# Kernel tuning notes

Hardware: AMD Instinct MI355X
Metric: run time of the kernel (lower is better)

## Reference

```python
import jax, jax.numpy as jnp
import numpy as np

HEADS = 16
HEAD_DIM = 64
DIM = 1024
INNER = HEADS * HEAD_DIM
EPS = 1e-5


def setup_inputs() -> dict:
    key = jax.random.key(0)
    ks = jax.random.split(key, 7)
    s_qkv = (2.0 / (DIM + 3 * INNER)) ** 0.5
    s_out = (2.0 / (INNER + DIM)) ** 0.5
    return {
        "x": jax.random.normal(ks[0], (4, 2048, DIM), dtype=jnp.float32),
        "w_qkv": jax.random.normal(ks[1], (DIM, 3 * INNER), dtype=jnp.float32) * s_qkv,
        "b_qkv": jnp.zeros((3 * INNER,), dtype=jnp.float32),
        "w_out": jax.random.normal(ks[2], (INNER, DIM), dtype=jnp.float32) * s_out,
        "b_out": jnp.zeros((DIM,), dtype=jnp.float32),
        "ln_gamma": jnp.ones((DIM,), dtype=jnp.float32),
        "ln_beta": jnp.zeros((DIM,), dtype=jnp.float32),
    }


def reference(x, w_qkv, b_qkv, w_out, b_out, ln_gamma, ln_beta):
    # Pre-norm LayerNorm
    mu = jnp.mean(x, axis=-1, keepdims=True)
    var = jnp.var(x, axis=-1, keepdims=True)
    xn = (x - mu) * jax.lax.rsqrt(var + EPS) * ln_gamma + ln_beta
    # QKV projection: [b, l, 3*inner]
    qkv = xn @ w_qkv + b_qkv
    q, k, v = jnp.split(qkv, 3, axis=-1)
    b, l, _ = x.shape
    def heads(t):  # [b, l, inner] -> [b, h, l, d]
        return t.reshape(b, l, HEADS, HEAD_DIM).transpose(0, 2, 1, 3)
    q, k, v = heads(q), heads(k), heads(v)
    scale = HEAD_DIM ** -0.5
    scores = jnp.einsum('bhqd,bhkd->bhqk', q, k) * scale
    att = jax.nn.softmax(scores, axis=-1)
    out = jnp.einsum('bhqk,bhkd->bhqd', att, v)
    out = out.transpose(0, 2, 1, 3).reshape(b, l, INNER)
    return out @ w_out + b_out
```

## Files before the change

### kernel.cpp

```cpp
#include <hip/hip_runtime.h>
#include <stdint.h>

typedef __bf16 bf16;
typedef bf16 bf16x4 __attribute__((ext_vector_type(4)));
typedef bf16 bf16x8 __attribute__((ext_vector_type(8)));
typedef float f32x4 __attribute__((ext_vector_type(4)));


__device__ __forceinline__ void gll16(const bf16* g, const bf16* l) {
  __builtin_amdgcn_global_load_lds(
      (__attribute__((address_space(1))) void*)(g),
      (__attribute__((address_space(3))) void*)(l),
      16, 0, 0);
}

__global__ __launch_bounds__(256) void ln_kernel(
    const float* __restrict__ x, const float* __restrict__ gamma,
    const float* __restrict__ beta, bf16* __restrict__ xn)
{
  __shared__ float red[8];
  const long row = blockIdx.x;
  const int t = threadIdx.x;
  f32x4 f = *(const f32x4*)(x + row * 1024 + t * 4);
  float sum = f[0] + f[1] + f[2] + f[3];
  float sq  = f[0]*f[0] + f[1]*f[1] + f[2]*f[2] + f[3]*f[3];
#pragma unroll
  for (int sh = 1; sh < 64; sh <<= 1) {
    sum += __shfl_xor(sum, sh, 64);
    sq  += __shfl_xor(sq,  sh, 64);
  }
  const int wave = t >> 6, lane = t & 63;
  if (lane == 0) { red[wave] = sum; red[wave + 4] = sq; }
  __syncthreads();
  sum = red[0] + red[1] + red[2] + red[3];
  sq  = red[4] + red[5] + red[6] + red[7];
  const float mu  = sum * (1.0f / 1024.0f);
  const float var = sq * (1.0f / 1024.0f) - mu * mu;
  const float rs  = rsqrtf(var + 1e-5f);
  f32x4 g = *(const f32x4*)(gamma + t * 4);
  f32x4 bb = *(const f32x4*)(beta + t * 4);
  bf16x4 ov;
#pragma unroll
  for (int i = 0; i < 4; i++)
    ov[i] = (bf16)((f[i] - mu) * rs * g[i] + bb[i]);
  *(bf16x4*)(xn + row * 1024 + t * 4) = ov;
}

__global__ __launch_bounds__(256) void transpose2_kernel(
    const float* __restrict__ wqkv, bf16* __restrict__ wqkvT,
    const float* __restrict__ wout, bf16* __restrict__ woutT)
{
  __shared__ bf16 tile[32][33];
  const int bx = blockIdx.x;
  const float* in;
  bf16* out;
  int Cc, c0;
  if (bx < 96) { in = wqkv; out = wqkvT; Cc = 3072; c0 = bx * 32; }
  else         { in = wout; out = woutT; Cc = 1024; c0 = (bx - 96) * 32; }
  const int r0 = blockIdx.y * 32;
  const int tx = threadIdx.x & 31, ty = threadIdx.x >> 5;
#pragma unroll
  for (int i = 0; i < 32; i += 8)
    tile[ty + i][tx] = (bf16)in[(long)(r0 + ty + i) * Cc + c0 + tx];
  __syncthreads();
#pragma unroll
  for (int i = 0; i < 32; i += 8)
    out[(long)(c0 + ty + i) * 1024 + r0 + tx] = tile[tx][ty + i];
}

__global__ __launch_bounds__(256, 3) void gemm_bt(
    const bf16* __restrict__ A, const bf16* __restrict__ BT,
    const float* __restrict__ bias, float* __restrict__ C,
    bf16* __restrict__ qb, bf16* __restrict__ kb, bf16* __restrict__ vtb,
    int K, int N, int mode)
{
  __shared__ bf16 sA[3][128 * 32];
  __shared__ bf16 sB[3][128 * 32];
  const int t = threadIdx.x;
  const int lane = t & 63;
  const int wave = t >> 6;
  const int wave_u = __builtin_amdgcn_readfirstlane(wave);
  const int quad = lane >> 4;
  const int c16 = lane & 15;
  const int wm = (wave >> 1) * 64;
  const int wn = (wave & 1) * 64;
  const int m0 = blockIdx.x * 128;
  const int n0 = blockIdx.y * 128;

  f32x4 acc[4][4] = {};

  const int srow = t >> 2;
  const int scol = (((t & 3) ^ ((t >> 3) & 3)) * 8);
  const bf16* gA = A + (long)(m0 + srow) * K + scol;
  const bf16* gB = BT + (long)(n0 + srow) * K + scol;
  const long rowskip = (long)64 * K;
  const int ksw = (quad ^ ((c16 >> 1) & 3)) * 8;

  const int S = K >> 5;

  auto stage = [&](int b, int kk) {
    const bf16* lA = sA[0] + b * 4096 + wave_u * 512;
    const bf16* lB = sB[0] + b * 4096 + wave_u * 512;
    const int k0 = kk * 32;
    gll16(gA + k0, lA);
    gll16(gA + k0 + rowskip, lA + 2048);
    gll16(gB + k0, lB);
    gll16(gB + k0 + rowskip, lB + 2048);
  };

  stage(0, 0);
  stage(1, 1);

  int bcur = 0;
  for (int s = 0; s < S; s++) {
    if (s + 2 < S) {
      const int bnx = (bcur >= 1) ? bcur - 1 : 2;
      stage(bnx, s + 2);
      asm volatile("s_waitcnt vmcnt(8)" ::: "memory");
    } else if (s + 1 < S) {
      asm volatile("s_waitcnt vmcnt(4)" ::: "memory");
    } else {
      asm volatile("s_waitcnt vmcnt(0)" ::: "memory");
    }
    __builtin_amdgcn_s_barrier();

    const bf16* cA = sA[0] + bcur * 4096;
    const bf16* cB = sB[0] + bcur * 4096;
    bf16x8 af[4], bfr[4];
#pragma unroll
    for (int i = 0; i < 4; i++)
      af[i] = *(const bf16x8*)(cA + (wm + i * 16 + c16) * 32 + ksw);
#pragma unroll
    for (int j = 0; j < 4; j++)
      bfr[j] = *(const bf16x8*)(cB + (wn + j * 16 + c16) * 32 + ksw);
#pragma unroll
    for (int i = 0; i < 4; i++)
#pragma unroll
      for (int j = 0; j < 4; j++)
        acc[i][j] = __builtin_amdgcn_mfma_f32_16x16x32_bf16(af[i], bfr[j], acc[i][j], 0, 0, 0);

    __builtin_amdgcn_s_barrier();
    bcur = (bcur == 2) ? 0 : bcur + 1;
  }

#pragma unroll
  for (int i = 0; i < 4; i++) {
    const int mbase = m0 + wm + i * 16 + quad * 4;
#pragma unroll
    for (int j = 0; j < 4; j++) {
      const int n = n0 + wn + j * 16 + c16;
      const float bv = bias[n];
      if (mode == 0) {
#pragma unroll
        for (int r = 0; r < 4; r++)
          C[(long)(mbase + r) * N + n] = acc[i][j][r] + bv;
      } else {
        const int part = n >> 10;
        const int inner = n & 1023;
        const int h = inner >> 6, d = inner & 63;
#pragma unroll
        for (int r = 0; r < 4; r++) {
          const int m = mbase + r;
          const int b = m >> 11, l = m & 2047;
          const long bh = (long)((b << 4) | h);
          const float v = acc[i][j][r] + bv;
          if (part == 0)      qb [(bh * 2048 + l) * 64 + d] = (bf16)(v * 0.18033688f);
          else if (part == 1) kb [(bh * 2048 + l) * 64 + d] = (bf16)v;
          else                vtb[(bh * 64 + d) * 2048 + l] = (bf16)v;
        }
      }
    }
  }
}

__global__ __launch_bounds__(256, 2) void attn_kernel(
    const bf16* __restrict__ q, const bf16* __restrict__ k,
    const bf16* __restrict__ vt, bf16* __restrict__ att)
{
  __shared__ bf16 sK[128 * 68];
  __shared__ bf16 sVt[64 * 132];

  const int i = blockIdx.x;
  const int xcd = i & 7;
  const int wi = i >> 3;
  const int qt = wi & 7;
  const int bh = xcd * 8 + (wi >> 3);
  const int b = bh >> 4, h = bh & 15;
  const int q0 = qt * 256;
  const int t = threadIdx.x;
  const int wave = t >> 6, lane = t & 63;
  const int quad = lane >> 4, c16 = lane & 15;

  const bf16* qp = q + (long)bh * (2048 * 64);
  const bf16* kp = k + (long)bh * (2048 * 64);
  const bf16* vp = vt + (long)bh * (64 * 2048);

  bf16x8 aq[4][2];
#pragma unroll
  for (int m = 0; m < 4; m++) {
    const bf16* qrow = qp + (long)(q0 + wave * 64 + m * 16 + c16) * 64 + quad * 8;
    aq[m][0] = *(const bf16x8*)(qrow);
    aq[m][1] = *(const bf16x8*)(qrow + 32);
  }

  f32x4 o_acc[4][4] = {};
  f32x4 o_sum[4] = {};
  bf16x8 vones;
#pragma unroll
  for (int z = 0; z < 8; z++) vones[z] = (bf16)1.0f;

  const int kr = t >> 3;
  const int kd = (t & 7) * 8;
  const int vr = t >> 4;
  const int vc = t & 15;
  const int vl = vc * 8;
  const int vD0 = (vc >> 2) * 32 + (vc & 1) * 16 + ((vc >> 1) & 1) * 4;

  bf16x8 kreg[4], vreg[4];
#pragma unroll
  for (int it = 0; it < 4; it++) {
    kreg[it] = *(const bf16x8*)(kp + (long)(it * 32 + kr) * 64 + kd);
    vreg[it] = *(const bf16x8*)(vp + (long)(it * 16 + vr) * 2048 + vl);
  }

  for (int kt = 0; kt < 16; kt++) {
    __syncthreads();
#pragma unroll
    for (int it = 0; it < 4; it++)
      *(bf16x8*)&sK[(it * 32 + kr) * 68 + kd] = kreg[it];
#pragma unroll
    for (int it = 0; it < 4; it++) {
      const bf16x8 v = vreg[it];
      const bf16x4 lo = __builtin_shufflevector(v, v, 0, 1, 2, 3);
      const bf16x4 hi = __builtin_shufflevector(v, v, 4, 5, 6, 7);
      bf16* d = &sVt[(it * 16 + vr) * 132 + vD0];
      *(bf16x4*)(d)     = lo;
      *(bf16x4*)(d + 8) = hi;
    }
    __syncthreads();

    const int kvn = ((kt + 1) & 15) * 128;

#pragma unroll
    for (int ks = 0; ks < 4; ks++) {
      bf16x8 ap[4];
#pragma unroll
      for (int e = 0; e < 2; e++) {
        const int jb = ks * 2 + e;
        const bf16x8 bk0 = *(const bf16x8*)&sK[(jb * 16 + c16) * 68 + quad * 8];
        const bf16x8 bk1 = *(const bf16x8*)&sK[(jb * 16 + c16) * 68 + 32 + quad * 8];
#pragma unroll
        for (int m = 0; m < 4; m++) {
          f32x4 z = {};
          z = __builtin_amdgcn_mfma_f32_16x16x32_bf16(bk0, aq[m][0], z, 0, 0, 0);
          z = __builtin_amdgcn_mfma_f32_16x16x32_bf16(bk1, aq[m][1], z, 0, 0, 0);
#pragma unroll
          for (int r = 0; r < 4; r++)
            ap[m][e * 4 + r] = (bf16)__builtin_amdgcn_exp2f(z[r]);
        }
      }
      if (ks == 1) {
#pragma unroll
        for (int it = 0; it < 4; it++)
          kreg[it] = *(const bf16x8*)(kp + (long)(kvn + it * 32 + kr) * 64 + kd);
      }
      if (ks == 2) {
#pragma unroll
        for (int it = 0; it < 4; it++)
          vreg[it] = *(const bf16x8*)(vp + (long)(it * 16 + vr) * 2048 + kvn + vl);
      }
#pragma unroll
      for (int m = 0; m < 4; m++)
        o_sum[m] = __builtin_amdgcn_mfma_f32_16x16x32_bf16(ap[m], vones, o_sum[m], 0, 0, 0);
#pragma unroll
      for (int jd = 0; jd < 4; jd++) {
        const bf16x8 bv = *(const bf16x8*)&sVt[(jd * 16 + c16) * 132 + ks * 32 + quad * 8];
#pragma unroll
        for (int m = 0; m < 4; m++)
          o_acc[m][jd] = __builtin_amdgcn_mfma_f32_16x16x32_bf16(ap[m], bv, o_acc[m][jd], 0, 0, 0);
      }
    }
  }

#pragma unroll
  for (int m = 0; m < 4; m++) {
#pragma unroll
    for (int r = 0; r < 4; r++) {
      const float inv = 1.0f / o_sum[m][r];
      const long rowbase = ((long)b * 2048 + q0 + wave * 64 + m * 16 + quad * 4 + r) * 1024 + h * 64;
#pragma unroll
      for (int jd = 0; jd < 4; jd++)
        att[rowbase + jd * 16 + c16] = (bf16)(o_acc[m][jd][r] * inv);
    }
  }
}

extern "C" void kernel_launch(void* const* d_in, const int* in_sizes, int n_in,
                              void* d_out, int out_size, void* d_ws, size_t ws_size,
                              hipStream_t stream) {
  (void)in_sizes; (void)n_in; (void)out_size; (void)ws_size;
  const float* x     = (const float*)d_in[0];
  const float* w_qkv = (const float*)d_in[1];
  const float* b_qkv = (const float*)d_in[2];
  const float* w_out = (const float*)d_in[3];
  const float* b_out = (const float*)d_in[4];
  const float* gamma = (const float*)d_in[5];
  const float* beta  = (const float*)d_in[6];
  float* out = (float*)d_out;
  bf16* ws  = (bf16*)d_ws;

  bf16* xn    = ws;
  bf16* wqkvT = ws + 8388608;
  bf16* woutT = wqkvT + 3145728;
  bf16* qbuf  = woutT + 1048576;
  bf16* kbuf  = qbuf + 8388608;
  bf16* vtbuf = kbuf + 8388608;
  bf16* att   = xn;

  transpose2_kernel<<<dim3(128, 32), 256, 0, stream>>>(w_qkv, wqkvT, w_out, woutT);
  ln_kernel<<<dim3(8192), 256, 0, stream>>>(x, gamma, beta, xn);
  gemm_bt<<<dim3(8192 / 128, 3072 / 128), 256, 0, stream>>>(
      xn, wqkvT, b_qkv, (float*)nullptr, qbuf, kbuf, vtbuf, 1024, 3072, 1);
  attn_kernel<<<dim3(512), 256, 0, stream>>>(qbuf, kbuf, vtbuf, att);
  gemm_bt<<<dim3(8192 / 128, 1024 / 128), 256, 0, stream>>>(
      att, woutT, b_out, out, (bf16*)nullptr, (bf16*)nullptr, (bf16*)nullptr, 1024, 1024, 0);
}
```

Baseline: 272.5 us.

## Add 256x256-tile 8-wave QKV GEMM with interleaved staging and MFMA scheduling

Replaces the 128x128 QKV projection GEMM with a dedicated kernel that uses 256x256 block tiles, 512 threads and a K-tile of 64. Global-to-LDS loads are double-buffered and interleaved with quarter-tile MFMA groups under explicit barriers, waitcnts and setprio. The aim is more operand reuse per LDS byte and better overlap of loads with matrix math. In exchange the grid shrinks to 384 blocks, the schedule is intricate to get right, and the scattered q/k/vT epilogue stores are unchanged.

```diff
diff --git a/kernel.cpp b/kernel.cpp
--- a/kernel.cpp
+++ b/kernel.cpp
@@ -71,8 +71,7 @@
 __global__ __launch_bounds__(256, 3) void gemm_bt(
     const bf16* __restrict__ A, const bf16* __restrict__ BT,
     const float* __restrict__ bias, float* __restrict__ C,
-    bf16* __restrict__ qb, bf16* __restrict__ kb, bf16* __restrict__ vtb,
-    int K, int N, int mode)
+    int K, int N)
 {
   __shared__ bf16 sA[3][128 * 32];
   __shared__ bf16 sB[3][128 * 32];
@@ -150,27 +149,168 @@
     for (int j = 0; j < 4; j++) {
       const int n = n0 + wn + j * 16 + c16;
       const float bv = bias[n];
-      if (mode == 0) {
-#pragma unroll
-        for (int r = 0; r < 4; r++)
-          C[(long)(mbase + r) * N + n] = acc[i][j][r] + bv;
-      } else {
-        const int part = n >> 10;
-        const int inner = n & 1023;
-        const int h = inner >> 6, d = inner & 63;
-#pragma unroll
-        for (int r = 0; r < 4; r++) {
-          const int m = mbase + r;
-          const int b = m >> 11, l = m & 2047;
-          const long bh = (long)((b << 4) | h);
-          const float v = acc[i][j][r] + bv;
-          if (part == 0)      qb [(bh * 2048 + l) * 64 + d] = (bf16)(v * 0.18033688f);
-          else if (part == 1) kb [(bh * 2048 + l) * 64 + d] = (bf16)v;
-          else                vtb[(bh * 64 + d) * 2048 + l] = (bf16)v;
-        }
+#pragma unroll
+      for (int r = 0; r < 4; r++)
+        C[(long)(mbase + r) * N + n] = acc[i][j][r] + bv;
+    }
+  }
+}
+
+__global__ __launch_bounds__(512, 2) void gemm_qkv256(
+    const bf16* __restrict__ A, const bf16* __restrict__ BT,
+    const float* __restrict__ bias,
+    bf16* __restrict__ qb, bf16* __restrict__ kb, bf16* __restrict__ vtb,
+    int K, int N)
+{
+  __shared__ bf16 sA[2][2][128 * 64];
+  __shared__ bf16 sB[2][2][128 * 64];
+  const int t = threadIdx.x;
+  const int lane = t & 63;
+  const int wave = t >> 6;
+  const int wave_u = __builtin_amdgcn_readfirstlane(wave);
+  const int quad = lane >> 4, c16 = lane & 15;
+  const int wM = wave >> 2;
+  const int wN = wave & 3;
+  const int wm = wM * 128;
+  const int wn = wN * 64;
+  const int m0 = blockIdx.x * 256;
+  const int n0 = blockIdx.y * 256;
+  const int NT = K >> 6;
+  const int NI = K >> 7;
+
+  f32x4 acc[8][4] = {};
+
+  const int sr = t >> 3;
+  const int scol = ((t & 7) ^ (sr & 7)) * 8;
+  const int fsw = c16 & 7;
+
+  auto stageA = [&](int buf, int half, int tile) {
+    const long kc = (long)tile * 64;
+    const long rb = (long)(m0 + half * 128);
+    const bf16* l = &sA[buf][half][0] + wave_u * 512;
+    gll16(A + (rb + sr) * K + kc + scol, l);
+    gll16(A + (rb + 64 + sr) * K + kc + scol, l + 4096);
+  };
+  auto stageB = [&](int buf, int half, int tile) {
+    const long kc = (long)tile * 64;
+    const long rb = (long)(n0 + half * 128);
+    const bf16* l = &sB[buf][half][0] + wave_u * 512;
+    gll16(BT + (rb + sr) * K + kc + scol, l);
+    gll16(BT + (rb + 64 + sr) * K + kc + scol, l + 4096);
+  };
+
+  bf16x8 af[4][2], bfr[4][2];
+  auto loadA = [&](int b, int mh) {
+#pragma unroll
+    for (int mi = 0; mi < 4; mi++) {
+      const int lr = (mh * 4 + mi) * 16 + c16;
+#pragma unroll
+      for (int ks = 0; ks < 2; ks++)
+        af[mi][ks] = *(const bf16x8*)&sA[b][wM][lr * 64 + (((ks * 4 + quad) ^ fsw) * 8)];
+    }
+  };
+  auto loadB = [&](int b) {
+#pragma unroll
+    for (int ni = 0; ni < 4; ni++) {
+      const int lr = (wN & 1) * 64 + ni * 16 + c16;
+#pragma unroll
+      for (int ks = 0; ks < 2; ks++)
+        bfr[ni][ks] = *(const bf16x8*)&sB[b][wN >> 1][lr * 64 + (((ks * 4 + quad) ^ fsw) * 8)];
+    }
+  };
+
+#define QUADMFMA(MH, NH)                                                      \
+  __builtin_amdgcn_s_setprio(1);                                              \
+  _Pragma("unroll")                                                           \
+  for (int mi = 0; mi < 4; mi++)                                              \
+    _Pragma("unroll")                                                         \
+    for (int ni = 0; ni < 2; ni++)                                            \
+      _Pragma("unroll")                                                       \
+      for (int ks = 0; ks < 2; ks++)                                          \
+        acc[(MH)*4 + mi][(NH)*2 + ni] = __builtin_amdgcn_mfma_f32_16x16x32_bf16( \
+            af[mi][ks], bfr[(NH)*2 + ni][ks], acc[(MH)*4 + mi][(NH)*2 + ni], 0, 0, 0); \
+  __builtin_amdgcn_s_setprio(0);
+
+#define LGKM_FENCE                                        \
+  asm volatile("s_waitcnt lgkmcnt(0)" ::: "memory");      \
+  __builtin_amdgcn_sched_barrier(0);
+
+  stageB(0, 0, 0); stageB(0, 1, 0); stageA(0, 0, 0); stageA(0, 1, 0);
+  stageB(1, 0, 1); stageB(1, 1, 1); stageA(1, 0, 1);
+
+  for (int i = 0; i < NI; i++) {
+    const int tb = (2 * i + 2 < NT) ? 2 * i + 2 : NT - 1;
+    const int tc = (2 * i + 3 < NT) ? 2 * i + 3 : NT - 1;
+
+    stageA(1, 1, 2 * i + 1);
+    asm volatile("s_waitcnt vmcnt(8)" ::: "memory");
+    __builtin_amdgcn_s_barrier();
+    loadA(0, 0); loadB(0);
+    QUADMFMA(0, 0)
+    LGKM_FENCE
+    __builtin_amdgcn_s_barrier();
+    stageB(0, 0, tb);
+    __builtin_amdgcn_s_barrier();
+    QUADMFMA(0, 1)
+    __builtin_amdgcn_s_barrier();
+    stageB(0, 1, tb);
+    __builtin_amdgcn_s_barrier();
+    loadA(0, 1);
+    QUADMFMA(1, 0)
+    LGKM_FENCE
+    __builtin_amdgcn_s_barrier();
+    stageA(0, 0, tb);
+    __builtin_amdgcn_s_barrier();
+    QUADMFMA(1, 1)
+    __builtin_amdgcn_s_barrier();
+    stageA(0, 1, tb);
+    asm volatile("s_waitcnt vmcnt(8)" ::: "memory");
+    __builtin_amdgcn_s_barrier();
+    loadA(1, 0); loadB(1);
+    QUADMFMA(0, 0)
+    LGKM_FENCE
+    __builtin_amdgcn_s_barrier();
+    stageB(1, 0, tc);
+    __builtin_amdgcn_s_barrier();
+    QUADMFMA(0, 1)
+    __builtin_amdgcn_s_barrier();
+    stageB(1, 1, tc);
+    __builtin_amdgcn_s_barrier();
+    loadA(1, 1);
+    QUADMFMA(1, 0)
+    LGKM_FENCE
+    __builtin_amdgcn_s_barrier();
+    stageA(1, 0, tc);
+    __builtin_amdgcn_s_barrier();
+    QUADMFMA(1, 1)
+    __builtin_amdgcn_s_barrier();
+  }
+  asm volatile("s_waitcnt vmcnt(0)" ::: "memory");
+
+#pragma unroll
+  for (int mi = 0; mi < 8; mi++) {
+    const int mbase = m0 + wm + mi * 16 + quad * 4;
+#pragma unroll
+    for (int ni = 0; ni < 4; ni++) {
+      const int n = n0 + wn + ni * 16 + c16;
+      const float bv = bias[n];
+      const int part = n >> 10;
+      const int inner = n & 1023;
+      const int h = inner >> 6, d = inner & 63;
+#pragma unroll
+      for (int r = 0; r < 4; r++) {
+        const int m = mbase + r;
+        const int b = m >> 11, l = m & 2047;
+        const long bh = (long)((b << 4) | h);
+        const float v = acc[mi][ni][r] + bv;
+        if (part == 0)      qb [(bh * 2048 + l) * 64 + d] = (bf16)(v * 0.18033688f);
+        else if (part == 1) kb [(bh * 2048 + l) * 64 + d] = (bf16)v;
+        else                vtb[(bh * 64 + d) * 2048 + l] = (bf16)v;
       }
     }
   }
+#undef QUADMFMA
+#undef LGKM_FENCE
 }
 
 __global__ __launch_bounds__(256, 2) void attn_kernel(
@@ -319,9 +459,9 @@
 
   transpose2_kernel<<<dim3(128, 32), 256, 0, stream>>>(w_qkv, wqkvT, w_out, woutT);
   ln_kernel<<<dim3(8192), 256, 0, stream>>>(x, gamma, beta, xn);
-  gemm_bt<<<dim3(8192 / 128, 3072 / 128), 256, 0, stream>>>(
-      xn, wqkvT, b_qkv, (float*)nullptr, qbuf, kbuf, vtbuf, 1024, 3072, 1);
+  gemm_qkv256<<<dim3(8192 / 256, 3072 / 256), 512, 0, stream>>>(
+      xn, wqkvT, b_qkv, qbuf, kbuf, vtbuf, 1024, 3072);
   attn_kernel<<<dim3(512), 256, 0, stream>>>(qbuf, kbuf, vtbuf, att);
   gemm_bt<<<dim3(8192 / 128, 1024 / 128), 256, 0, stream>>>(
-      att, woutT, b_out, out, (bf16*)nullptr, (bf16*)nullptr, (bf16*)nullptr, 1024, 1024, 0);
-}
+      att, woutT, b_out, out, 1024, 1024);
+}
```

Result: slower. 283.4 us (+4.0%).
